# Kernel tuning notes

Measured on AMD Instinct MI355X. Metric: run time of the kernel, lower is better.

Reference implementation:

```python
import jax, jax.numpy as jnp
import numpy as np

TEXT_DIM, GIN = 5000, 128
B, N, E = 4096, 200000, 6400000
AE_HID, AE_EMB, G_HID, G_EMB = 8, 4, 8, 4


def _gcn(x, W, b, src, dst):
    N_ = x.shape[0]
    h = x @ W
    loop = jnp.arange(N_)
    s = jnp.concatenate([src, loop])
    d = jnp.concatenate([dst, loop])
    deg = jax.ops.segment_sum(jnp.ones(s.shape[0], h.dtype), d, num_segments=N_)
    dinv = jnp.where(deg > 0, jax.lax.rsqrt(jnp.maximum(deg, 1e-12)), 0.0)
    norm = dinv[s] * dinv[d]
    out = jax.ops.segment_sum(h[s] * norm[:, None], d, num_segments=N_)
    return out + b


def setup_inputs() -> dict:
    key = jax.random.key(0)
    ks = jax.random.split(key, 20)
    def lin(k, fan_in, fan_out):
        lim = 1.0 / np.sqrt(fan_in)
        kw, kb = jax.random.split(k)
        W = jax.random.uniform(kw, (fan_in, fan_out), jnp.float32, -lim, lim)
        b = jax.random.uniform(kb, (fan_out,), jnp.float32, -lim, lim)
        return W, b
    W_e1, b_e1 = lin(ks[0], TEXT_DIM, AE_HID)
    W_e2, b_e2 = lin(ks[1], AE_HID, AE_EMB)
    W_d1, b_d1 = lin(ks[2], AE_EMB, AE_HID)
    W_d2, b_d2 = lin(ks[3], AE_HID, TEXT_DIM)
    W_g1, b_g1 = lin(ks[4], GIN, G_HID)
    W_g2, b_g2 = lin(ks[5], G_HID, G_EMB)
    W_c, b_c = lin(ks[6], AE_EMB + G_EMB, 1)
    text_x = jax.random.normal(ks[7], (B, TEXT_DIM), jnp.float32)
    node_x = jax.random.normal(ks[8], (N, GIN), jnp.float32)
    edge_index = jax.random.randint(ks[9], (2, E), 0, N, jnp.int64 if jax.config.jax_enable_x64 else jnp.int32)
    batch = jnp.sort(jax.random.randint(ks[10], (N,), 0, B, edge_index.dtype))
    return {"text_x": text_x, "node_x": node_x, "edge_index": edge_index, "batch": batch,
            "W_e1": W_e1, "b_e1": b_e1, "W_e2": W_e2, "b_e2": b_e2,
            "W_d1": W_d1, "b_d1": b_d1, "W_d2": W_d2, "b_d2": b_d2,
            "W_g1": W_g1, "b_g1": b_g1, "W_g2": W_g2, "b_g2": b_g2,
            "W_c": W_c, "b_c": b_c}


def reference(text_x, node_x, edge_index, batch,
              W_e1, b_e1, W_e2, b_e2, W_d1, b_d1, W_d2, b_d2,
              W_g1, b_g1, W_g2, b_g2, W_c, b_c):
    # Autoencoder (eval mode: dropout = identity)
    z_text = jax.nn.relu(jax.nn.relu(text_x @ W_e1 + b_e1) @ W_e2 + b_e2)
    x_hat = jax.nn.sigmoid(jax.nn.relu(z_text @ W_d1 + b_d1) @ W_d2 + b_d2)
    # GNN encoder
    src, dst = edge_index[0], edge_index[1]
    h = jax.nn.relu(_gcn(node_x, W_g1, b_g1, src, dst))
    h = _gcn(h, W_g2, b_g2, src, dst)
    # global mean pool over graphs
    nb = text_x.shape[0]
    sums = jax.ops.segment_sum(h, batch, num_segments=nb)
    cnt = jax.ops.segment_sum(jnp.ones(h.shape[0], h.dtype), batch, num_segments=nb)
    z_graph = sums / jnp.maximum(cnt, 1.0)[:, None]
    z = jnp.concatenate([z_text, z_graph], axis=1)
    logits = z @ W_c + b_c
    return (x_hat, logits, z)
```

## Files before the change

### kernel.cpp

```cpp
#include <hip/hip_runtime.h>

#define BB 4096
#define TD 5000
#define NN 200000
#define EE 6400000
#define NBK 782

__global__ void k_init(const int* __restrict__ e, unsigned int* __restrict__ deg,
                       int* __restrict__ flag) {
    int i = blockIdx.x * 256 + threadIdx.x;
    if (i < NN) deg[i] = 1u;
    if (blockIdx.x == 0) {
        __shared__ int r[256];
        int tid = threadIdx.x;
        int acc = 0;
        for (int k = tid; k < 4096; k += 256) acc |= e[2 * k + 1];
        r[tid] = acc;
        __syncthreads();
        for (int s = 128; s > 0; s >>= 1) {
            if (tid < s) r[tid] |= r[tid + s];
            __syncthreads();
        }
        if (tid == 0) *flag = (r[0] == 0) ? 1 : 0;
    }
}

__global__ void k_rank(const int* __restrict__ edge, const int* __restrict__ flag,
                       unsigned int* __restrict__ deg, unsigned int* __restrict__ r) {
    int e = blockIdx.x * 256 + threadIdx.x;
    if (e >= EE) return;
    int f = *flag;
    int d = f ? edge[2 * (EE + e)] : edge[EE + e];
    r[e] = atomicAdd(&deg[d], 1u);
}

__global__ void kA_all(const unsigned int* __restrict__ deg, float* __restrict__ dinv,
                       unsigned int* __restrict__ bsum, const int* __restrict__ batch,
                       const int* __restrict__ flag, unsigned int* __restrict__ bnd) {
    __shared__ unsigned int s[256];
    int tid = threadIdx.x;
    int i = blockIdx.x * 256 + tid;
    unsigned int c = 0u;
    if (i < NN) {
        unsigned int u = deg[i];
        dinv[i] = rsqrtf((float)u);
        c = u - 1u;
        int fg = *flag;
        int b = fg ? batch[2 * i] : batch[i];
        int bp = (i == 0) ? -1 : (fg ? batch[2 * (i - 1)] : batch[i - 1]);
        for (int bb = bp + 1; bb <= b; bb++) bnd[bb] = (unsigned int)i;
        if (i == NN - 1)
            for (int bb = b + 1; bb <= BB; bb++) bnd[bb] = (unsigned int)NN;
    }
    s[tid] = c;
    __syncthreads();
    for (int st = 128; st > 0; st >>= 1) {
        if (tid < st) s[tid] += s[tid + st];
        __syncthreads();
    }
    if (tid == 0) bsum[blockIdx.x] = s[0];
}

__global__ void kB_scanblocks(const unsigned int* __restrict__ bsum, unsigned int* __restrict__ bpre,
                              unsigned int* __restrict__ indptr) {
    __shared__ unsigned int s[1024];
    int t = threadIdx.x;
    s[t] = (t < NBK) ? bsum[t] : 0u;
    __syncthreads();
    for (int off = 1; off < 1024; off <<= 1) {
        unsigned int v = (t >= off) ? s[t - off] : 0u;
        __syncthreads();
        s[t] += v;
        __syncthreads();
    }
    if (t < NBK) bpre[t] = (t == 0) ? 0u : s[t - 1];
    if (t == 0) indptr[NN] = EE;
}

__global__ void kC_indptr(const unsigned int* __restrict__ deg, const unsigned int* __restrict__ bpre,
                          unsigned int* __restrict__ indptr) {
    __shared__ unsigned int s[256];
    int tid = threadIdx.x;
    int i = blockIdx.x * 256 + tid;
    unsigned int c = (i < NN) ? (deg[i] - 1u) : 0u;
    s[tid] = c;
    __syncthreads();
    for (int off = 1; off < 256; off <<= 1) {
        unsigned int v = (tid >= off) ? s[tid - off] : 0u;
        __syncthreads();
        s[tid] += v;
        __syncthreads();
    }
    if (i < NN) indptr[i] = bpre[blockIdx.x] + s[tid] - c;
}

__global__ void k_place(const int* __restrict__ edge, const int* __restrict__ flag,
                        const unsigned int* __restrict__ indptr, const unsigned int* __restrict__ r,
                        int* __restrict__ csr_src) {
    int e = blockIdx.x * 256 + threadIdx.x;
    if (e >= EE) return;
    int f = *flag;
    int s = f ? edge[2 * e] : edge[e];
    int d = f ? edge[2 * (EE + e)] : edge[EE + e];
    csr_src[indptr[d] + r[e] - 1u] = s;
}

__global__ __launch_bounds__(256) void k_gcn1_mm(
    const float* __restrict__ nodex, const float* __restrict__ Wg1,
    const float* __restrict__ dinv, float* __restrict__ h0g)
{
    __shared__ float W[128 * 8];
    int tid = threadIdx.x;
    for (int i = tid; i < 1024; i += 256) W[i] = Wg1[i];
    __syncthreads();
    int row = blockIdx.x * 256 + tid;
    if (row >= NN) return;
    const float4* xr = (const float4*)(nodex + (size_t)row * 128);
    float acc[8];
#pragma unroll
    for (int j = 0; j < 8; j++) acc[j] = 0.f;
#pragma unroll 8
    for (int c = 0; c < 32; c++) {
        float4 v = xr[c];
        const float* wr = &W[c * 32];
#pragma unroll
        for (int j = 0; j < 8; j++)
            acc[j] += v.x * wr[j] + v.y * wr[8 + j] + v.z * wr[16 + j] + v.w * wr[24 + j];
    }
    float di = dinv[row];
    float* o = h0g + (size_t)row * 8;
#pragma unroll
    for (int j = 0; j < 8; j++) o[j] = di * acc[j];
}

__global__ __launch_bounds__(256) void k_gather1(
    const unsigned int* __restrict__ indptr, const int* __restrict__ csr_src,
    const float* __restrict__ h0g, const float* __restrict__ dinv,
    const float* __restrict__ bg1, const float* __restrict__ Wg2,
    float* __restrict__ h2g)
{
    __shared__ float W[32];
    __shared__ float b1[8];
    __shared__ float h1s[4][8];
    int tid = threadIdx.x;
    if (tid < 32) W[tid] = Wg2[tid];
    if (tid < 8) b1[tid] = bg1[tid];
    __syncthreads();
    int wid = tid >> 6, lane = tid & 63;
    int i = blockIdx.x * 4 + wid;
    if (i < NN) {
        int beg = indptr[i], end = indptr[i + 1];
        int f = lane & 7;
        float a = 0.f;
        for (int k = beg + (lane >> 3); k < end; k += 8)
            a += h0g[(size_t)csr_src[k] * 8 + f];
        a += __shfl_xor(a, 8, 64);
        a += __shfl_xor(a, 16, 64);
        a += __shfl_xor(a, 32, 64);
        if (lane < 8) {
            float di = dinv[i];
            h1s[wid][f] = fmaxf(di * (a + h0g[(size_t)i * 8 + f]) + b1[f], 0.f);
        }
    }
    __syncthreads();
    if (i < NN && lane < 4) {
        float di = dinv[i];
        float s = 0.f;
#pragma unroll
        for (int k = 0; k < 8; k++) s += h1s[wid][k] * W[k * 4 + lane];
        h2g[(size_t)i * 4 + lane] = di * s;
    }
}

__global__ __launch_bounds__(256) void k_gather2(
    const unsigned int* __restrict__ indptr, const int* __restrict__ csr_src,
    const float* __restrict__ h2g, const float* __restrict__ dinv,
    const float* __restrict__ bg2, float* __restrict__ h2f)
{
    __shared__ float b2[4];
    int tid = threadIdx.x;
    if (tid < 4) b2[tid] = bg2[tid];
    __syncthreads();
    int wid = tid >> 6, lane = tid & 63;
    int i = blockIdx.x * 4 + wid;
    if (i >= NN) return;
    int beg = indptr[i], end = indptr[i + 1];
    int f = lane & 3;
    float a = 0.f;
    for (int k = beg + (lane >> 2); k < end; k += 16)
        a += h2g[(size_t)csr_src[k] * 4 + f];
    a += __shfl_xor(a, 4, 64);
    a += __shfl_xor(a, 8, 64);
    a += __shfl_xor(a, 16, 64);
    a += __shfl_xor(a, 32, 64);
    if (lane < 4) {
        float di = dinv[i];
        h2f[(size_t)i * 4 + f] = di * (a + h2g[(size_t)i * 4 + f]) + b2[f];
    }
}

__global__ __launch_bounds__(256) void k_ae_encode(
    const float* __restrict__ text,
    const float* __restrict__ We1, const float* __restrict__ be1,
    const float* __restrict__ We2, const float* __restrict__ be2,
    float* __restrict__ z_text)
{
    __shared__ float red[8][256];
    __shared__ float t1[8];
    int row = blockIdx.x, tid = threadIdx.x;
    const float4* xrow = (const float4*)(text + (size_t)row * TD);
    float acc[8];
#pragma unroll
    for (int j = 0; j < 8; j++) acc[j] = 0.f;
    for (int v = tid; v < 1250; v += 256) {
        float4 xv = xrow[v];
        const float4* w = (const float4*)(We1 + (size_t)v * 32);
        float xc[4] = {xv.x, xv.y, xv.z, xv.w};
#pragma unroll
        for (int c = 0; c < 4; c++) {
            float4 wa = w[c * 2], wb = w[c * 2 + 1];
            acc[0] += xc[c] * wa.x; acc[1] += xc[c] * wa.y;
            acc[2] += xc[c] * wa.z; acc[3] += xc[c] * wa.w;
            acc[4] += xc[c] * wb.x; acc[5] += xc[c] * wb.y;
            acc[6] += xc[c] * wb.z; acc[7] += xc[c] * wb.w;
        }
    }
#pragma unroll
    for (int j = 0; j < 8; j++) red[j][tid] = acc[j];
    __syncthreads();
    for (int s = 128; s > 0; s >>= 1) {
        if (tid < s) {
#pragma unroll
            for (int j = 0; j < 8; j++) red[j][tid] += red[j][tid + s];
        }
        __syncthreads();
    }
    if (tid < 8) t1[tid] = fmaxf(red[tid][0] + be1[tid], 0.f);
    __syncthreads();
    if (tid < 4) {
        float z = be2[tid];
#pragma unroll
        for (int k = 0; k < 8; k++) z += t1[k] * We2[k * 4 + tid];
        z_text[row * 4 + tid] = fmaxf(z, 0.f);
    }
}

__global__ __launch_bounds__(256) void k_final(
    const float* __restrict__ h2f, const unsigned int* __restrict__ bnd,
    const float* __restrict__ z_text, const float* __restrict__ Wc,
    const float* __restrict__ bc, float* __restrict__ out_logits,
    float* __restrict__ out_z)
{
    __shared__ float red[256][4];
    int g = blockIdx.x, tid = threadIdx.x;
    int lo = bnd[g], hi = bnd[g + 1];
    float a0 = 0.f, a1 = 0.f, a2 = 0.f, a3 = 0.f;
    for (int i = lo + tid; i < hi; i += 256) {
        float4 v = *(const float4*)(h2f + (size_t)i * 4);
        a0 += v.x; a1 += v.y; a2 += v.z; a3 += v.w;
    }
    red[tid][0] = a0; red[tid][1] = a1; red[tid][2] = a2; red[tid][3] = a3;
    __syncthreads();
    for (int s = 128; s > 0; s >>= 1) {
        if (tid < s) {
            red[tid][0] += red[tid + s][0]; red[tid][1] += red[tid + s][1];
            red[tid][2] += red[tid + s][2]; red[tid][3] += red[tid + s][3];
        }
        __syncthreads();
    }
    if (tid == 0) {
        float c = (float)(hi - lo);
        c = fmaxf(c, 1.f);
        float z8[8];
#pragma unroll
        for (int j = 0; j < 4; j++) z8[j] = z_text[g * 4 + j];
#pragma unroll
        for (int j = 0; j < 4; j++) z8[4 + j] = red[0][j] / c;
        float l = bc[0];
#pragma unroll
        for (int k = 0; k < 8; k++) l += z8[k] * Wc[k];
        out_logits[g] = l;
#pragma unroll
        for (int k = 0; k < 8; k++) out_z[g * 8 + k] = z8[k];
    }
}

__global__ __launch_bounds__(256) void k_ae_decode(
    const float* __restrict__ out_z,
    const float* __restrict__ Wd1, const float* __restrict__ bd1,
    const float* __restrict__ Wd2, const float* __restrict__ bd2,
    float* __restrict__ xhat)
{
    int row = blockIdx.x, tid = threadIdx.x;
    float zz[4];
#pragma unroll
    for (int j = 0; j < 4; j++) zz[j] = out_z[row * 8 + j];
    float t[8];
#pragma unroll
    for (int k = 0; k < 8; k++) {
        float s = bd1[k];
#pragma unroll
        for (int j = 0; j < 4; j++) s += zz[j] * Wd1[j * 8 + k];
        t[k] = fmaxf(s, 0.f);
    }
    float4* orow = (float4*)(xhat + (size_t)row * TD);
    for (int c4 = tid; c4 < 1250; c4 += 256) {
        float4 s = *(const float4*)(bd2 + c4 * 4);
#pragma unroll
        for (int k = 0; k < 8; k++) {
            float4 w = *(const float4*)(Wd2 + (size_t)k * TD + c4 * 4);
            s.x += t[k] * w.x; s.y += t[k] * w.y;
            s.z += t[k] * w.z; s.w += t[k] * w.w;
        }
        s.x = 1.f / (1.f + expf(-s.x));
        s.y = 1.f / (1.f + expf(-s.y));
        s.z = 1.f / (1.f + expf(-s.z));
        s.w = 1.f / (1.f + expf(-s.w));
        orow[c4] = s;
    }
}

extern "C" void kernel_launch(void* const* d_in, const int* in_sizes, int n_in,
                              void* d_out, int out_size, void* d_ws, size_t ws_size,
                              hipStream_t stream) {
    const float* text  = (const float*)d_in[0];
    const float* nodex = (const float*)d_in[1];
    const int* edge    = (const int*)d_in[2];
    const int* batch   = (const int*)d_in[3];
    const float* We1 = (const float*)d_in[4];
    const float* be1 = (const float*)d_in[5];
    const float* We2 = (const float*)d_in[6];
    const float* be2 = (const float*)d_in[7];
    const float* Wd1 = (const float*)d_in[8];
    const float* bd1 = (const float*)d_in[9];
    const float* Wd2 = (const float*)d_in[10];
    const float* bd2 = (const float*)d_in[11];
    const float* Wg1 = (const float*)d_in[12];
    const float* bg1 = (const float*)d_in[13];
    const float* Wg2 = (const float*)d_in[14];
    const float* bg2 = (const float*)d_in[15];
    const float* Wc  = (const float*)d_in[16];
    const float* bc  = (const float*)d_in[17];

    char* sc = (char*)d_out;
    float*        h0g    = (float*)(sc + 0);
    float*        h2g    = (float*)(sc + 6400000);
    float*        h2f    = (float*)(sc + 9600000);
    float*        dinv   = (float*)(sc + 12800000);
    unsigned int* deg    = (unsigned int*)(sc + 13600000);
    unsigned int* indptr = (unsigned int*)(sc + 14400000);
    unsigned int* rnk    = (unsigned int*)(sc + 15200004);
    int*          csr    = (int*)(sc + 40800004);
    unsigned int* bsum   = (unsigned int*)(sc + 66400004);
    unsigned int* bpre   = (unsigned int*)(sc + 66403132);
    float*        z_text = (float*)(sc + 66406260);
    unsigned int* bnd    = (unsigned int*)(sc + 66471796);
    int*          flag   = (int*)(sc + 66488184);

    float* out_xhat   = (float*)d_out;
    float* out_logits = out_xhat + (size_t)BB * TD;
    float* out_z      = out_logits + BB;

    const int NB_E = EE / 256;
    const int NB_G = (NN + 3) / 4;

    k_init<<<NBK, 256, 0, stream>>>(edge, deg, flag);
    k_rank<<<NB_E, 256, 0, stream>>>(edge, flag, deg, rnk);
    kA_all<<<NBK, 256, 0, stream>>>(deg, dinv, bsum, batch, flag, bnd);
    kB_scanblocks<<<1, 1024, 0, stream>>>(bsum, bpre, indptr);
    kC_indptr<<<NBK, 256, 0, stream>>>(deg, bpre, indptr);
    k_place<<<NB_E, 256, 0, stream>>>(edge, flag, indptr, rnk, csr);

    k_gcn1_mm<<<NBK, 256, 0, stream>>>(nodex, Wg1, dinv, h0g);
    k_gather1<<<NB_G, 256, 0, stream>>>(indptr, csr, h0g, dinv, bg1, Wg2, h2g);
    k_gather2<<<NB_G, 256, 0, stream>>>(indptr, csr, h2g, dinv, bg2, h2f);

    k_ae_encode<<<BB, 256, 0, stream>>>(text, We1, be1, We2, be2, z_text);
    k_final<<<BB, 256, 0, stream>>>(h2f, bnd, z_text, Wc, bc, out_logits, out_z);
    k_ae_decode<<<BB, 256, 0, stream>>>(out_z, Wd1, bd1, Wd2, bd2, out_xhat);
}
```

Measured before the change: 782.8 us.

## Co-schedule atomic degree ranking with text encoder in one interleaved kernel

Merges the edge-rank atomic kernel and the autoencoder encode kernel into one launch. Rank blocks and encode blocks are interleaved so the latency-bound atomics overlap with the bandwidth-bound text GEMV. Each rank and place thread now handles 8 or 4 edges with batched loads to raise memory-level parallelism. This costs more register and LDS pressure for the rank blocks, which share the launch with the encoder's shared arrays.

```diff
diff --git a/kernel.cpp b/kernel.cpp
--- a/kernel.cpp
+++ b/kernel.cpp
@@ -25,13 +25,78 @@
     }
 }
 
-__global__ void k_rank(const int* __restrict__ edge, const int* __restrict__ flag,
-                       unsigned int* __restrict__ deg, unsigned int* __restrict__ r) {
-    int e = blockIdx.x * 256 + threadIdx.x;
-    if (e >= EE) return;
-    int f = *flag;
-    int d = f ? edge[2 * (EE + e)] : edge[EE + e];
-    r[e] = atomicAdd(&deg[d], 1u);
+__global__ __launch_bounds__(256) void k_rank_enc(
+    const int* __restrict__ edge, const int* __restrict__ flag,
+    unsigned int* __restrict__ deg, unsigned int* __restrict__ rnk,
+    const float* __restrict__ text,
+    const float* __restrict__ We1, const float* __restrict__ be1,
+    const float* __restrict__ We2, const float* __restrict__ be2,
+    float* __restrict__ z_text)
+{
+    __shared__ float red[8][256];
+    __shared__ float t1[8];
+    int bid = blockIdx.x, tid = threadIdx.x;
+    int enc_id = -1, rank_id = -1;
+    if (bid < 6250) {
+        if (bid & 1) enc_id = bid >> 1;
+        else rank_id = bid >> 1;
+    } else {
+        enc_id = 3125 + (bid - 6250);
+    }
+
+    if (rank_id >= 0) {
+        int f = *flag;
+        int base = rank_id * 2048 + tid;
+        int d[8];
+#pragma unroll
+        for (int k = 0; k < 8; k++) {
+            int e = base + k * 256;
+            d[k] = f ? edge[2 * (EE + e)] : edge[EE + e];
+        }
+        unsigned int rr[8];
+#pragma unroll
+        for (int k = 0; k < 8; k++) rr[k] = atomicAdd(&deg[d[k]], 1u);
+#pragma unroll
+        for (int k = 0; k < 8; k++) rnk[base + k * 256] = rr[k];
+        return;
+    }
+
+    int row = enc_id;
+    const float4* xrow = (const float4*)(text + (size_t)row * TD);
+    float acc[8];
+#pragma unroll
+    for (int j = 0; j < 8; j++) acc[j] = 0.f;
+    for (int v = tid; v < 1250; v += 256) {
+        float4 xv = xrow[v];
+        const float4* w = (const float4*)(We1 + (size_t)v * 32);
+        float xc[4] = {xv.x, xv.y, xv.z, xv.w};
+#pragma unroll
+        for (int c = 0; c < 4; c++) {
+            float4 wa = w[c * 2], wb = w[c * 2 + 1];
+            acc[0] += xc[c] * wa.x; acc[1] += xc[c] * wa.y;
+            acc[2] += xc[c] * wa.z; acc[3] += xc[c] * wa.w;
+            acc[4] += xc[c] * wb.x; acc[5] += xc[c] * wb.y;
+            acc[6] += xc[c] * wb.z; acc[7] += xc[c] * wb.w;
+        }
+    }
+#pragma unroll
+    for (int j = 0; j < 8; j++) red[j][tid] = acc[j];
+    __syncthreads();
+    for (int s = 128; s > 0; s >>= 1) {
+        if (tid < s) {
+#pragma unroll
+            for (int j = 0; j < 8; j++) red[j][tid] += red[j][tid + s];
+        }
+        __syncthreads();
+    }
+    if (tid < 8) t1[tid] = fmaxf(red[tid][0] + be1[tid], 0.f);
+    __syncthreads();
+    if (tid < 4) {
+        float z = be2[tid];
+#pragma unroll
+        for (int k = 0; k < 8; k++) z += t1[k] * We2[k * 4 + tid];
+        z_text[row * 4 + tid] = fmaxf(z, 0.f);
+    }
 }
 
 __global__ void kA_all(const unsigned int* __restrict__ deg, float* __restrict__ dinv,
@@ -95,14 +160,25 @@
 }
 
 __global__ void k_place(const int* __restrict__ edge, const int* __restrict__ flag,
-                        const unsigned int* __restrict__ indptr, const unsigned int* __restrict__ r,
-                        int* __restrict__ csr_src) {
-    int e = blockIdx.x * 256 + threadIdx.x;
-    if (e >= EE) return;
+                        const unsigned int* __restrict__ indptr, const unsigned int* __restrict__ rnk,
+                        int* __restrict__ csr) {
     int f = *flag;
-    int s = f ? edge[2 * e] : edge[e];
-    int d = f ? edge[2 * (EE + e)] : edge[EE + e];
-    csr_src[indptr[d] + r[e] - 1u] = s;
+    int base = blockIdx.x * 1024 + threadIdx.x;
+    int s[4], d[4];
+#pragma unroll
+    for (int k = 0; k < 4; k++) {
+        int e = base + k * 256;
+        s[k] = f ? edge[2 * e] : edge[e];
+        d[k] = f ? edge[2 * (EE + e)] : edge[EE + e];
+    }
+    unsigned int rr[4];
+#pragma unroll
+    for (int k = 0; k < 4; k++) rr[k] = rnk[base + k * 256];
+    unsigned int ip[4];
+#pragma unroll
+    for (int k = 0; k < 4; k++) ip[k] = indptr[d[k]];
+#pragma unroll
+    for (int k = 0; k < 4; k++) csr[ip[k] + rr[k] - 1u] = s[k];
 }
 
 __global__ __launch_bounds__(256) void k_gcn1_mm(
@@ -196,52 +272,6 @@
     if (lane < 4) {
         float di = dinv[i];
         h2f[(size_t)i * 4 + f] = di * (a + h2g[(size_t)i * 4 + f]) + b2[f];
-    }
-}
-
-__global__ __launch_bounds__(256) void k_ae_encode(
-    const float* __restrict__ text,
-    const float* __restrict__ We1, const float* __restrict__ be1,
-    const float* __restrict__ We2, const float* __restrict__ be2,
-    float* __restrict__ z_text)
-{
-    __shared__ float red[8][256];
-    __shared__ float t1[8];
-    int row = blockIdx.x, tid = threadIdx.x;
-    const float4* xrow = (const float4*)(text + (size_t)row * TD);
-    float acc[8];
-#pragma unroll
-    for (int j = 0; j < 8; j++) acc[j] = 0.f;
-    for (int v = tid; v < 1250; v += 256) {
-        float4 xv = xrow[v];
-        const float4* w = (const float4*)(We1 + (size_t)v * 32);
-        float xc[4] = {xv.x, xv.y, xv.z, xv.w};
-#pragma unroll
-        for (int c = 0; c < 4; c++) {
-            float4 wa = w[c * 2], wb = w[c * 2 + 1];
-            acc[0] += xc[c] * wa.x; acc[1] += xc[c] * wa.y;
-            acc[2] += xc[c] * wa.z; acc[3] += xc[c] * wa.w;
-            acc[4] += xc[c] * wb.x; acc[5] += xc[c] * wb.y;
-            acc[6] += xc[c] * wb.z; acc[7] += xc[c] * wb.w;
-        }
-    }
-#pragma unroll
-    for (int j = 0; j < 8; j++) red[j][tid] = acc[j];
-    __syncthreads();
-    for (int s = 128; s > 0; s >>= 1) {
-        if (tid < s) {
-#pragma unroll
-            for (int j = 0; j < 8; j++) red[j][tid] += red[j][tid + s];
-        }
-        __syncthreads();
-    }
-    if (tid < 8) t1[tid] = fmaxf(red[tid][0] + be1[tid], 0.f);
-    __syncthreads();
-    if (tid < 4) {
-        float z = be2[tid];
-#pragma unroll
-        for (int k = 0; k < 8; k++) z += t1[k] * We2[k * 4 + tid];
-        z_text[row * 4 + tid] = fmaxf(z, 0.f);
     }
 }
 
@@ -361,21 +391,18 @@
     float* out_logits = out_xhat + (size_t)BB * TD;
     float* out_z      = out_logits + BB;
 
-    const int NB_E = EE / 256;
-    const int NB_G = (NN + 3) / 4;
-
     k_init<<<NBK, 256, 0, stream>>>(edge, deg, flag);
-    k_rank<<<NB_E, 256, 0, stream>>>(edge, flag, deg, rnk);
+    k_rank_enc<<<7221, 256, 0, stream>>>(edge, flag, deg, rnk,
+                                         text, We1, be1, We2, be2, z_text);
     kA_all<<<NBK, 256, 0, stream>>>(deg, dinv, bsum, batch, flag, bnd);
     kB_scanblocks<<<1, 1024, 0, stream>>>(bsum, bpre, indptr);
     kC_indptr<<<NBK, 256, 0, stream>>>(deg, bpre, indptr);
-    k_place<<<NB_E, 256, 0, stream>>>(edge, flag, indptr, rnk, csr);
+    k_place<<<6250, 256, 0, stream>>>(edge, flag, indptr, rnk, csr);
 
     k_gcn1_mm<<<NBK, 256, 0, stream>>>(nodex, Wg1, dinv, h0g);
-    k_gather1<<<NB_G, 256, 0, stream>>>(indptr, csr, h0g, dinv, bg1, Wg2, h2g);
-    k_gather2<<<NB_G, 256, 0, stream>>>(indptr, csr, h2g, dinv, bg2, h2f);
-
-    k_ae_encode<<<BB, 256, 0, stream>>>(text, We1, be1, We2, be2, z_text);
+    k_gather1<<<(NN + 3) / 4, 256, 0, stream>>>(indptr, csr, h0g, dinv, bg1, Wg2, h2g);
+    k_gather2<<<(NN + 3) / 4, 256, 0, stream>>>(indptr, csr, h2g, dinv, bg2, h2f);
+
     k_final<<<BB, 256, 0, stream>>>(h2f, bnd, z_text, Wc, bc, out_logits, out_z);
     k_ae_decode<<<BB, 256, 0, stream>>>(out_z, Wd1, bd1, Wd2, bd2, out_xhat);
 }
```

Measured after the change: 723.1 us. 7.6% less time.
